# Performance work log

Measured on AMD Instinct MI355X. Metric: run time of the kernel, lower is better.

## Reference

```python
import jax, jax.numpy as jnp
import numpy as np
from jax import lax

B, C, H, W = 4, 256, 64, 64
R1, R2 = 4, 8


def conv1x1(x, w, b):
    # x: [B,C,H,W], w: [O,C], b: [O]
    return jnp.einsum('bchw,oc->bohw', x, w) + b[None, :, None, None]


def dwconv3x3(x, w, b):
    # depthwise 3x3, SAME padding. w: [C,1,3,3]
    y = lax.conv_general_dilated(x, w, window_strides=(1, 1), padding='SAME',
                                 dimension_numbers=('NCHW', 'OIHW', 'NCHW'),
                                 feature_group_count=x.shape[1])
    return y + b[None, :, None, None]


def setup_inputs() -> dict:
    key = jax.random.key(0)
    ks = jax.random.split(key, 20)
    s = 0.02
    inp = {
        'x':   jax.random.normal(ks[0], (B, C, H, W), jnp.float32),
        'Wq':  jax.random.normal(ks[1], (C, C), jnp.float32) * s,
        'bq':  jnp.zeros((C,), jnp.float32),
        'Wk':  jax.random.normal(ks[2], (C, 1, 3, 3), jnp.float32) * s,
        'bk':  jnp.zeros((C,), jnp.float32),
        'Wv':  jax.random.normal(ks[3], (C, 1, 3, 3), jnp.float32) * s,
        'bv':  jnp.zeros((C,), jnp.float32),
        'Wl':  jax.random.normal(ks[4], (C, 1, 3, 3), jnp.float32) * s,
        'bl':  jnp.zeros((C,), jnp.float32),
        'Ws1': jax.random.normal(ks[5], (C // R1, C), jnp.float32) * s,
        'bs1': jnp.zeros((C // R1,), jnp.float32),
        'Ws2': jax.random.normal(ks[6], (C, C // R1), jnp.float32) * s,
        'bs2': jnp.zeros((C,), jnp.float32),
        'Wc1': jax.random.normal(ks[7], (C // R2, C), jnp.float32) * s,
        'bc1': jnp.zeros((C // R2,), jnp.float32),
        'Wc2': jax.random.normal(ks[8], (C, C // R2), jnp.float32) * s,
        'bc2': jnp.zeros((C,), jnp.float32),
        'Wo':  jax.random.normal(ks[9], (C, C), jnp.float32) * s,
        'bo':  jnp.zeros((C,), jnp.float32),
    }
    return inp


def reference(x, Wq, bq, Wk, bk, Wv, bv, Wl, bl, Ws1, bs1, Ws2, bs2,
              Wc1, bc1, Wc2, bc2, Wo, bo):
    b_, c_, h_, w_ = x.shape
    hw = h_ * w_
    scale = jnp.sqrt(jnp.float32(c_))

    q = conv1x1(x, Wq, bq).reshape(b_, c_, hw).transpose(0, 2, 1)   # [B,HW,C]
    k = dwconv3x3(x, Wk, bk).reshape(b_, c_, hw)                    # [B,C,HW]
    v_img = dwconv3x3(x, Wv, bv)                                    # [B,C,H,W]
    v = v_img.reshape(b_, c_, hw).transpose(0, 2, 1)                # [B,HW,C]

    attn = jax.nn.softmax(jnp.einsum('bnc,bcm->bnm', q, k) / scale, axis=-1)
    global_out = jnp.einsum('bnm,bmc->bnc', attn, v)                # [B,HW,C]
    global_out = global_out.transpose(0, 2, 1).reshape(b_, c_, h_, w_)

    local_out = dwconv3x3(v_img, Wl, bl)                            # [B,C,H,W]

    spatial_weight = jax.nn.sigmoid(
        conv1x1(jax.nn.relu(conv1x1(local_out, Ws1, bs1)), Ws2, bs2))

    gap = jnp.mean(global_out, axis=(2, 3), keepdims=True)          # [B,C,1,1]
    channel_weight = jax.nn.sigmoid(
        conv1x1(jax.nn.relu(conv1x1(gap, Wc1, bc1)), Wc2, bc2))     # [B,C,1,1]

    fused = global_out * channel_weight + local_out * spatial_weight
    return conv1x1(fused, Wo, bo) + x
```

## Files before the change

### kernel.cpp

```cpp
#include <hip/hip_runtime.h>
#include <hip/hip_fp8.h>
#include <stdint.h>

typedef unsigned short u16;
typedef unsigned char u8;
typedef __attribute__((ext_vector_type(8))) __bf16 bf16x8;
typedef __attribute__((ext_vector_type(8))) short short8s;
typedef __attribute__((ext_vector_type(4))) float float4v;
typedef __attribute__((ext_vector_type(16))) float floatx16;
typedef __attribute__((ext_vector_type(4))) int int4v;
typedef __attribute__((ext_vector_type(8))) int int8v;

static constexpr int NB = 4, NC = 256, NH = 64, NW = 64, NHW = 4096;
static constexpr int BC = 64;
static constexpr int NKV = 4;
static constexpr int KVCHUNK = NHW / NKV;

static constexpr size_t MB = 1ull << 20;
static constexpr size_t OFF_KBF    = 0;
static constexpr size_t OFF_LBF    = 8 * MB;
static constexpr size_t OFF_GT     = 0;
static constexpr size_t OFF_XT     = 16 * MB;
static constexpr size_t OFF_LPART  = 16 * MB;
static constexpr size_t OFF_FUSEDT = 16 * MB;
static constexpr size_t OFF_QT8    = 24 * MB;
static constexpr size_t OFF_KT8    = 32 * MB;
static constexpr size_t OFF_V8     = 40 * MB;
static constexpr size_t OFF_LT     = 48 * MB;
static constexpr size_t OFF_OPART  = 56 * MB;
static constexpr size_t OFF_HIDT   = 88 * MB;
static constexpr size_t OFF_GAP    = OFF_HIDT + 2 * MB;
static constexpr size_t OFF_WQB    = OFF_GAP + 8 * 1024;
static constexpr size_t OFF_WS1B   = OFF_WQB + 131072;
static constexpr size_t OFF_WS2B   = OFF_WS1B + 32768;
static constexpr size_t OFF_WOB    = OFF_WS2B + 32768;

__device__ __forceinline__ float b2f(u16 h) {
    union { float f; unsigned u; } v; v.u = ((unsigned)h) << 16; return v.f;
}
__device__ __forceinline__ u16 f2b(float f) {
    union { float f; unsigned u; } v; v.f = f;
    unsigned r = v.u + 0x7fffu + ((v.u >> 16) & 1u);
    return (u16)(r >> 16);
}
__device__ __forceinline__ u8 f2f8(float f) {
    __hip_fp8_e4m3 h(f);
    return *reinterpret_cast<u8*>(&h);
}

__device__ __forceinline__ void load_lds16(const void* gsrc, void* ldst) {
    __builtin_amdgcn_global_load_lds(
        (__attribute__((address_space(1))) void*)(uintptr_t)gsrc,
        (__attribute__((address_space(3))) void*)ldst,
        16, 0, 0);
}

__global__ __launch_bounds__(256) void prep(
    const float* __restrict__ x,
    const float* __restrict__ Wq, const float* __restrict__ Ws1,
    const float* __restrict__ Ws2, const float* __restrict__ Wo,
    const float* __restrict__ Wk, const float* __restrict__ bk,
    const float* __restrict__ Wv, const float* __restrict__ bv,
    const float* __restrict__ Wl, const float* __restrict__ bl,
    u16* __restrict__ Wqb, u16* __restrict__ Ws1b, u16* __restrict__ Ws2b, u16* __restrict__ Wob,
    float* __restrict__ gap,
    u16* __restrict__ k_bf, u8* __restrict__ vN8, u16* __restrict__ local_bf,
    u16* __restrict__ xT)
{
    __shared__ __align__(16) unsigned char pshm[9216];
    const int bid = blockIdx.x;
    const int t = threadIdx.x;

    if (bid < 644) {
        int id = bid * 256 + t;
        if (id < 65536)        Wqb[id] = f2b(Wq[id]);
        else if (id < 81920)   Ws1b[id - 65536] = f2b(Ws1[id - 65536]);
        else if (id < 98304)   Ws2b[id - 81920] = f2b(Ws2[id - 81920]);
        else if (id < 163840)  Wob[id - 98304] = f2b(Wo[id - 98304]);
        else if (id < 164864)  gap[id - 163840] = 0.f;
        return;
    }
    if (bid < 2692) {
        int l = bid - 644;
        int xx0 = t & 63, cl = t >> 6;
        int y0 = (l & 7) * 8;
        int c  = ((l >> 3) & 63) * 4 + cl;
        int b  = l >> 9;
        const float* xb = x + ((size_t)b * NC + c) * NHW;
        float wk[9], wv[9], wl[9];
#pragma unroll
        for (int i = 0; i < 9; i++) { wk[i] = Wk[c*9+i]; wv[i] = Wv[c*9+i]; wl[i] = Wl[c*9+i]; }
        float bkc = bk[c], bvc = bv[c], blc = bl[c];

        auto ldx = [&](int y) -> float {
            return ((unsigned)y <= 63u) ? xb[y * 64 + xx0] : 0.f;
        };
        auto conv3 = [&](const float* w9, float a, float bm, float cc) -> float {
            float au = __shfl_up(a, 1, 64),   ad = __shfl_down(a, 1, 64);
            float bu = __shfl_up(bm, 1, 64),  bd = __shfl_down(bm, 1, 64);
            float cu = __shfl_up(cc, 1, 64),  cd = __shfl_down(cc, 1, 64);
            float al = (xx0 == 0) ? 0.f : au, ar = (xx0 == 63) ? 0.f : ad;
            float bl_ = (xx0 == 0) ? 0.f : bu, br = (xx0 == 63) ? 0.f : bd;
            float cle = (xx0 == 0) ? 0.f : cu, cr = (xx0 == 63) ? 0.f : cd;
            return w9[0]*al + w9[1]*a  + w9[2]*ar
                 + w9[3]*bl_ + w9[4]*bm + w9[5]*br
                 + w9[6]*cle + w9[7]*cc + w9[8]*cr;
        };

        float xm2 = ldx(y0 - 2), xm1 = ldx(y0 - 1), x0v = ldx(y0), xp1 = ldx(y0 + 1);
        float vm1 = (y0 - 1 >= 0) ? (bvc + conv3(wv, xm2, xm1, x0v)) : 0.f;
        float v0  = bvc + conv3(wv, xm1, x0v, xp1);

        size_t base = ((size_t)b * NC + c) * NHW;
#pragma unroll
        for (int yi = 0; yi < 8; yi++) {
            int y = y0 + yi;
            float xp2 = ldx(y + 2);
            float vp1 = (y + 1 <= 63) ? (bvc + conv3(wv, x0v, xp1, xp2)) : 0.f;
            float kk  = bkc + conv3(wk, xm1, x0v, xp1);
            float ll  = blc + conv3(wl, vm1, v0, vp1);
            size_t o = base + y * 64 + xx0;
            k_bf[o]     = f2b(kk);
            vN8[o]      = f2f8(v0);
            local_bf[o] = f2b(ll);
            xm1 = x0v; x0v = xp1; xp1 = xp2;
            vm1 = v0;  v0 = vp1;
        }
        return;
    }
    {
        u16 (*tile)[72] = reinterpret_cast<u16 (*)[72]>(pshm);
        int l = bid - 2692;
        int n0 = (l & 63) * 64;
        int c0 = ((l >> 6) & 3) * 64;
        int b  = l >> 8;
        const float* src = x + (size_t)b * NC * NHW;
        u16* dst = xT + (size_t)b * NHW * NC;
        int c = t >> 2, nb = (t & 3) * 16;
#pragma unroll
        for (int q = 0; q < 4; q++) {
            float4 v = *(const float4*)(src + (size_t)(c0 + c) * NHW + n0 + nb + q * 4);
            tile[c][nb + q * 4 + 0] = f2b(v.x);
            tile[c][nb + q * 4 + 1] = f2b(v.y);
            tile[c][nb + q * 4 + 2] = f2b(v.z);
            tile[c][nb + q * 4 + 3] = f2b(v.w);
        }
        __syncthreads();
        int cl = t & 63, ng = t >> 6;
#pragma unroll
        for (int j = 0; j < 16; j++) {
            int n = ng * 16 + j;
            dst[(size_t)(n0 + n) * NC + c0 + cl] = tile[cl][n];
        }
    }
}

__global__ __launch_bounds__(256) void mid(
    const u16* __restrict__ k_bf, const u16* __restrict__ local_bf,
    u8* __restrict__ kT8, u16* __restrict__ localT,
    const u16* __restrict__ xT, const u16* __restrict__ Wqb, const float* __restrict__ bq,
    u8* __restrict__ qT8)
{
    __shared__ __align__(16) u16 tile[64][72];
    const int t = threadIdx.x;
    const int bid = blockIdx.x;
    if (bid < 2048) {
        int n0 = (bid & 63) * 64, c0 = ((bid >> 6) & 3) * 64;
        int zb = bid >> 8, b = zb >> 1;
        const u16* src = (zb & 1) ? local_bf : k_bf;
        src += (size_t)b * NC * NHW;
        int c = t >> 2, nb = (t & 3) * 16;
        *(short8s*)&tile[c][nb]     = *(const short8s*)(src + (size_t)(c0 + c) * NHW + n0 + nb);
        *(short8s*)&tile[c][nb + 8] = *(const short8s*)(src + (size_t)(c0 + c) * NHW + n0 + nb + 8);
        __syncthreads();
        int cl = t & 63, ng = t >> 6;
        if (zb & 1) {
            u16* dst = localT + (size_t)b * NHW * NC;
#pragma unroll
            for (int j = 0; j < 16; j++) {
                int n = ng * 16 + j;
                dst[(size_t)(n0 + n) * NC + c0 + cl] = tile[cl][n];
            }
        } else {
            u8* dst = kT8 + (size_t)b * NHW * NC;
#pragma unroll
            for (int j = 0; j < 16; j++) {
                int n = ng * 16 + j;
                dst[(size_t)(n0 + n) * NC + c0 + cl] = f2f8(b2f(tile[cl][n]));
            }
        }
        return;
    }
    {
        const int w = t >> 6, lane = t & 63;
        const int lm = lane & 15, quad = lane >> 4;
        const int l = bid - 2048;
        const int b = l >> 7;
        const int s_base = (l & 127) * 32 + (w & 1) * 16;
        const int ch = (w >> 1) * 128;
        const u16* xTb = xT + (size_t)b * NHW * NC;
        u8* qTb = qT8 + (size_t)b * NHW * NC;
        bf16x8 aq[8];
#pragma unroll
        for (int kt = 0; kt < 8; kt++)
            aq[kt] = *(const bf16x8*)(xTb + (size_t)(s_base + lm) * NC + kt * 32 + quad * 8);
        float4v acc[8];
#pragma unroll
        for (int j = 0; j < 8; j++) acc[j] = (float4v){0.f, 0.f, 0.f, 0.f};
#pragma unroll
        for (int kt = 0; kt < 8; kt++) {
#pragma unroll
            for (int j = 0; j < 8; j++) {
                bf16x8 bw = *(const bf16x8*)(Wqb + (size_t)(ch + j * 16 + lm) * 256 + kt * 32 + quad * 8);
                acc[j] = __builtin_amdgcn_mfma_f32_16x16x32_bf16(aq[kt], bw, acc[j], 0, 0, 0);
            }
        }
#pragma unroll
        for (int j = 0; j < 8; j++) {
            int cout = ch + j * 16 + lm;
            float bb = bq[cout];
#pragma unroll
            for (int r = 0; r < 4; r++) {
                int s = s_base + quad * 4 + r;
                qTb[(size_t)s * NC + cout] = f2f8(acc[j][r] + bb);
            }
        }
    }
}

__device__ __forceinline__ void stage_tiles(
    const u8* __restrict__ kb, const u8* __restrict__ vb8, int kv0,
    u8* KlB, u8* VlB, int w, int lane)
{
#pragma unroll
    for (int i = 0; i < 4; i++) {
        int g = (w * 4 + i) * 64 + lane;
        int n = g >> 4, jj = g & 15, cc = jj ^ (n & 15);
        load_lds16(kb + (size_t)(kv0 + n) * NC + cc * 16, KlB + (w * 4 + i) * 1024);
    }
#pragma unroll
    for (int i = 0; i < 4; i++) {
        int g = (w * 4 + i) * 64 + lane;
        int c = g >> 2, hh = g & 3;
        int sc = hh ^ ((c >> 1) & 3);
        load_lds16(vb8 + (size_t)c * NHW + kv0 + sc * 16, VlB + (w * 4 + i) * 1024);
    }
}

__global__ __launch_bounds__(256, 2) void attn_hid(
    const u8* __restrict__ qT8, const u8* __restrict__ kT8,
    const u8* __restrict__ vN8, u8* __restrict__ Opart8, float* __restrict__ lpart,
    const u16* __restrict__ localT, const u16* __restrict__ Ws1b, const float* __restrict__ bs1,
    u16* __restrict__ hidT)
{
    __shared__ __align__(16) u8 Kl[2][BC * 256];
    __shared__ __align__(16) u8 Vl[2][256 * BC];

    const int t = threadIdx.x;
    const int w = t >> 6, lane = t & 63;

    if (blockIdx.x >= 512) {
        const int lm = lane & 15, quad = lane >> 4;
        const int l = blockIdx.x - 512;
        const int b = l >> 7;
        const int s_base = (l & 127) * 32 + (w & 1) * 16;
        const int ch = (w >> 1) * 32;
        const u16* lTb = localT + (size_t)b * NHW * NC;
        u16* hTb = hidT + (size_t)b * NHW * 64;
        bf16x8 ah[8];
#pragma unroll
        for (int kt = 0; kt < 8; kt++)
            ah[kt] = *(const bf16x8*)(lTb + (size_t)(s_base + lm) * NC + kt * 32 + quad * 8);
        float4v acc[2];
#pragma unroll
        for (int j = 0; j < 2; j++) acc[j] = (float4v){0.f, 0.f, 0.f, 0.f};
#pragma unroll
        for (int kt = 0; kt < 8; kt++) {
#pragma unroll
            for (int j = 0; j < 2; j++) {
                bf16x8 bw = *(const bf16x8*)(Ws1b + (size_t)(ch + j * 16 + lm) * 256 + kt * 32 + quad * 8);
                acc[j] = __builtin_amdgcn_mfma_f32_16x16x32_bf16(ah[kt], bw, acc[j], 0, 0, 0);
            }
        }
#pragma unroll
        for (int j = 0; j < 2; j++) {
            int h = ch + j * 16 + lm;
            float bb = bs1[h];
#pragma unroll
            for (int r = 0; r < 4; r++) {
                int s = s_base + quad * 4 + r;
                hTb[(size_t)s * 64 + h] = f2b(fmaxf(acc[j][r] + bb, 0.0f));
            }
        }
        return;
    }

    const int combo = blockIdx.x & 15;
    const int b  = combo >> 2;
    const int jc = combo & 3;
    const int n0 = (blockIdx.x >> 4) * 128;
    const int lr = lane & 31, l5 = lane >> 5;
    const int m4 = lr & 15;
    const int scl = (int)0x7F7F7F7F;

    const u8* qb = qT8 + (size_t)b * NHW * NC;
    const u8* kb = kT8 + (size_t)b * NHW * NC;
    const u8* vb8 = vN8 + (size_t)b * NC * NHW;

    int8v aqm[4];
    {
        int qrow = n0 + w * 32 + lr;
#pragma unroll
        for (int ks = 0; ks < 4; ks++)
            aqm[ks] = *(const int8v*)(qb + (size_t)qrow * NC + ks * 64 + l5 * 32);
    }

    floatx16 oacc[8];
#pragma unroll
    for (int i = 0; i < 8; i++)
#pragma unroll
        for (int j = 0; j < 16; j++) oacc[i][j] = 0.f;
    float lsum = 0.f;

    const int kvbeg = jc * KVCHUNK;
    stage_tiles(kb, vb8, kvbeg, Kl[0], Vl[0], w, lane);

    int buf = 0;
#pragma unroll 1
    for (int it = 0; it < KVCHUNK / BC; it++) {
        const int nxt = (it + 1 < KVCHUNK / BC) ? (kvbeg + (it + 1) * BC) : kvbeg;
        stage_tiles(kb, vb8, nxt, Kl[buf ^ 1], Vl[buf ^ 1], w, lane);
        asm volatile("s_waitcnt vmcnt(8)" ::: "memory");
        __builtin_amdgcn_s_barrier();

        const u8* KlB = Kl[buf];
        const u8* VlB = Vl[buf];

        unsigned uA0, uA1, uA2, uA3, uB0, uB1, uB2, uB3;

        {
            floatx16 sacc;
#pragma unroll
            for (int j = 0; j < 16; j++) sacc[j] = 0.f;
            __builtin_amdgcn_s_setprio(1);
#pragma unroll
            for (int ks = 0; ks < 4; ks++) {
                int e = ks * 4 + l5 * 2;
                int4v klo = *(const int4v*)&KlB[lr * 256 + ((e ^ m4) * 16)];
                int4v khi = *(const int4v*)&KlB[lr * 256 + (((e + 1) ^ m4) * 16)];
                int8v ka = __builtin_shufflevector(klo, khi, 0, 1, 2, 3, 4, 5, 6, 7);
                sacc = __builtin_amdgcn_mfma_scale_f32_32x32x64_f8f6f4(
                    ka, aqm[ks], sacc, 0, 0, 0, scl, 0, scl);
            }
            __builtin_amdgcn_s_setprio(0);
            float p[16];
#pragma unroll
            for (int r = 0; r < 16; r++)
                p[r] = __expf(sacc[r] * 0.0625f);
            float s0 = (p[0] + p[1]) + (p[2] + p[3]);
            float s1 = (p[4] + p[5]) + (p[6] + p[7]);
            float s2 = (p[8] + p[9]) + (p[10] + p[11]);
            float s3 = (p[12] + p[13]) + (p[14] + p[15]);
            lsum += (s0 + s1) + (s2 + s3);
            uA0 = __builtin_amdgcn_cvt_pk_fp8_f32(p[0], p[1], 0, false);
            uA0 = __builtin_amdgcn_cvt_pk_fp8_f32(p[2], p[3], uA0, true);
            uA1 = __builtin_amdgcn_cvt_pk_fp8_f32(p[4], p[5], 0, false);
            uA1 = __builtin_amdgcn_cvt_pk_fp8_f32(p[6], p[7], uA1, true);
            uA2 = __builtin_amdgcn_cvt_pk_fp8_f32(p[8], p[9], 0, false);
            uA2 = __builtin_amdgcn_cvt_pk_fp8_f32(p[10], p[11], uA2, true);
            uA3 = __builtin_amdgcn_cvt_pk_fp8_f32(p[12], p[13], 0, false);
            uA3 = __builtin_amdgcn_cvt_pk_fp8_f32(p[14], p[15], uA3, true);
        }
        {
            floatx16 sacc;
#pragma unroll
            for (int j = 0; j < 16; j++) sacc[j] = 0.f;
            __builtin_amdgcn_s_setprio(1);
#pragma unroll
            for (int ks = 0; ks < 4; ks++) {
                int e = ks * 4 + l5 * 2;
                int4v klo = *(const int4v*)&KlB[(32 + lr) * 256 + ((e ^ m4) * 16)];
                int4v khi = *(const int4v*)&KlB[(32 + lr) * 256 + (((e + 1) ^ m4) * 16)];
                int8v ka = __builtin_shufflevector(klo, khi, 0, 1, 2, 3, 4, 5, 6, 7);
                sacc = __builtin_amdgcn_mfma_scale_f32_32x32x64_f8f6f4(
                    ka, aqm[ks], sacc, 0, 0, 0, scl, 0, scl);
            }
            __builtin_amdgcn_s_setprio(0);
            float p[16];
#pragma unroll
            for (int r = 0; r < 16; r++)
                p[r] = __expf(sacc[r] * 0.0625f);
            float s0 = (p[0] + p[1]) + (p[2] + p[3]);
            float s1 = (p[4] + p[5]) + (p[6] + p[7]);
            float s2 = (p[8] + p[9]) + (p[10] + p[11]);
            float s3 = (p[12] + p[13]) + (p[14] + p[15]);
            lsum += (s0 + s1) + (s2 + s3);
            uB0 = __builtin_amdgcn_cvt_pk_fp8_f32(p[0], p[1], 0, false);
            uB0 = __builtin_amdgcn_cvt_pk_fp8_f32(p[2], p[3], uB0, true);
            uB1 = __builtin_amdgcn_cvt_pk_fp8_f32(p[4], p[5], 0, false);
            uB1 = __builtin_amdgcn_cvt_pk_fp8_f32(p[6], p[7], uB1, true);
            uB2 = __builtin_amdgcn_cvt_pk_fp8_f32(p[8], p[9], 0, false);
            uB2 = __builtin_amdgcn_cvt_pk_fp8_f32(p[10], p[11], uB2, true);
            uB3 = __builtin_amdgcn_cvt_pk_fp8_f32(p[12], p[13], 0, false);
            uB3 = __builtin_amdgcn_cvt_pk_fp8_f32(p[14], p[15], uB3, true);
        }
        asm volatile("v_permlane32_swap_b32 %0, %1" : "+v"(uA0), "+v"(uB0));
        asm volatile("v_permlane32_swap_b32 %0, %1" : "+v"(uA1), "+v"(uB1));
        asm volatile("v_permlane32_swap_b32 %0, %1" : "+v"(uA2), "+v"(uB2));
        asm volatile("v_permlane32_swap_b32 %0, %1" : "+v"(uA3), "+v"(uB3));
        int8v pa = {(int)uA0, (int)uB0, (int)uA1, (int)uB1,
                    (int)uA2, (int)uB2, (int)uA3, (int)uB3};

        __builtin_amdgcn_s_setprio(1);
#pragma unroll
        for (int ct = 0; ct < 8; ct++) {
            int c = ct * 32 + lr;
            int sw = (c >> 1) & 3;
            int4v v0 = *(const int4v*)&VlB[c * 64 + (((l5 * 2) ^ sw) * 16)];
            int4v v1 = *(const int4v*)&VlB[c * 64 + (((l5 * 2 + 1) ^ sw) * 16)];
            int8v bv = __builtin_shufflevector(v0, v1, 0, 1, 2, 3, 4, 5, 6, 7);
            oacc[ct] = __builtin_amdgcn_mfma_scale_f32_32x32x64_f8f6f4(
                pa, bv, oacc[ct], 0, 0, 0, scl, 0, scl);
        }
        __builtin_amdgcn_s_setprio(0);
        __builtin_amdgcn_s_barrier();
        buf ^= 1;
    }

    lsum += __shfl_xor(lsum, 32, 64);
    u8* Ob = Opart8 + ((size_t)(b * NKV + jc) * NHW + n0 + w * 32) * NC;
#pragma unroll
    for (int reg = 0; reg < 16; reg++) {
        int row = (reg & 3) + 8 * (reg >> 2) + 4 * l5;
#pragma unroll
        for (int ct = 0; ct < 8; ct++)
            Ob[(size_t)row * NC + ct * 32 + lr] = f2f8(oacc[ct][reg]);
    }
    if (lane < 32)
        lpart[(size_t)(b * NKV + jc) * NHW + n0 + w * 32 + lr] = lsum;
}

__global__ __launch_bounds__(256) void attn_combine(
    const u8* __restrict__ Opart8, const float* __restrict__ lpart,
    u16* __restrict__ gT, float* __restrict__ gap)
{
    __shared__ float gsum[256];
    int t = threadIdx.x;
    gsum[t] = 0.f;
    __syncthreads();
    int b = blockIdx.y;
    int n = blockIdx.x * 8 + (t >> 5);
    int c0 = (t & 31) * 8;
    float acc[8] = {};
    float l = 0.f;
#pragma unroll
    for (int j = 0; j < NKV; j++) {
        const u8* op = Opart8 + ((size_t)(b * NKV + j) * NHW + n) * NC + c0;
        unsigned long long v = *(const unsigned long long*)op;
        unsigned lo = (unsigned)v, hi = (unsigned)(v >> 32);
        acc[0] += __builtin_amdgcn_cvt_f32_fp8(lo, 0);
        acc[1] += __builtin_amdgcn_cvt_f32_fp8(lo, 1);
        acc[2] += __builtin_amdgcn_cvt_f32_fp8(lo, 2);
        acc[3] += __builtin_amdgcn_cvt_f32_fp8(lo, 3);
        acc[4] += __builtin_amdgcn_cvt_f32_fp8(hi, 0);
        acc[5] += __builtin_amdgcn_cvt_f32_fp8(hi, 1);
        acc[6] += __builtin_amdgcn_cvt_f32_fp8(hi, 2);
        acc[7] += __builtin_amdgcn_cvt_f32_fp8(hi, 3);
        l += lpart[(size_t)(b * NKV + j) * NHW + n];
    }
    float inv = 1.0f / l;
#pragma unroll
    for (int i = 0; i < 8; i++) acc[i] *= inv;
    short8s vo;
#pragma unroll
    for (int i = 0; i < 8; i++) ((u16*)&vo)[i] = f2b(acc[i]);
    *(short8s*)(gT + ((size_t)b * NHW + n) * NC + c0) = vo;
#pragma unroll
    for (int i = 0; i < 8; i++) atomicAdd(&gsum[c0 + i], acc[i]);
    __syncthreads();
    atomicAdd(&gap[b * NC + t], gsum[t]);
}

__global__ __launch_bounds__(256) void gemm_swfused_mfma(
    const u16* __restrict__ hidT, const u16* __restrict__ Ws2b, const float* __restrict__ bs2,
    const u16* __restrict__ gT, const u16* __restrict__ localT,
    const float* __restrict__ gap,
    const float* __restrict__ Wc1, const float* __restrict__ bc1,
    const float* __restrict__ Wc2, const float* __restrict__ bc2,
    u16* __restrict__ fusedT)
{
    __shared__ float g[256], h1[32], cwl[256];
    __shared__ float ph[32][9];
    const int t = threadIdx.x, w = t >> 6, lane = t & 63;
    const int lm = lane & 15, quad = lane >> 4;
    const int b = blockIdx.y;

    g[t] = gap[b * 256 + t] * (1.0f / 4096.0f);
    __syncthreads();
    {
        int h = t & 31, part = t >> 5;
        float s = 0.f;
        for (int c = part * 32; c < part * 32 + 32; c++) s += Wc1[h * 256 + c] * g[c];
        ph[h][part] = s;
    }
    __syncthreads();
    if (t < 32) {
        float s = bc1[t];
#pragma unroll
        for (int p = 0; p < 8; p++) s += ph[t][p];
        h1[t] = fmaxf(s, 0.f);
    }
    __syncthreads();
    {
        float s = bc2[t];
#pragma unroll
        for (int j = 0; j < 32; j++) s += Wc2[t * 32 + j] * h1[j];
        cwl[t] = 1.0f / (1.0f + __expf(-s));
    }
    __syncthreads();

    const int s_base = blockIdx.x * 32 + (w & 1) * 16;
    const int ch = (w >> 1) * 128;
    const u16* hTb = hidT + (size_t)b * NHW * 64;
    const u16* lTb = localT + (size_t)b * NHW * NC;
    const u16* gTb = gT + (size_t)b * NHW * NC;
    u16* fTb = fusedT + (size_t)b * NHW * NC;

    bf16x8 aq[2];
#pragma unroll
    for (int kt = 0; kt < 2; kt++)
        aq[kt] = *(const bf16x8*)(hTb + (size_t)(s_base + lm) * 64 + kt * 32 + quad * 8);

    float4v acc[8];
#pragma unroll
    for (int j = 0; j < 8; j++) acc[j] = (float4v){0.f, 0.f, 0.f, 0.f};

#pragma unroll
    for (int kt = 0; kt < 2; kt++) {
#pragma unroll
        for (int j = 0; j < 8; j++) {
            bf16x8 bw = *(const bf16x8*)(Ws2b + (size_t)(ch + j * 16 + lm) * 64 + kt * 32 + quad * 8);
            acc[j] = __builtin_amdgcn_mfma_f32_16x16x32_bf16(aq[kt], bw, acc[j], 0, 0, 0);
        }
    }
#pragma unroll
    for (int j = 0; j < 8; j++) {
        int c = ch + j * 16 + lm;
        float bb = bs2[c];
        float cwv = cwl[c];
#pragma unroll
        for (int r = 0; r < 4; r++) {
            int s = s_base + quad * 4 + r;
            float sw = 1.0f / (1.0f + __expf(-(acc[j][r] + bb)));
            float gg = b2f(gTb[(size_t)s * NC + c]);
            float lo = b2f(lTb[(size_t)s * NC + c]);
            fTb[(size_t)s * NC + c] = f2b(gg * cwv + lo * sw);
        }
    }
}

__global__ __launch_bounds__(256) void gemm_out_mfma(
    const u16* __restrict__ Wob, const u16* __restrict__ fusedT, const float* __restrict__ bo,
    const float* __restrict__ x, float* __restrict__ out)
{
    const int t = threadIdx.x, w = t >> 6, lane = t & 63;
    const int lm = lane & 15, quad = lane >> 4;
    const int b = blockIdx.z;
    const int o_base = blockIdx.x * 32 + (w & 1) * 16;
    const int n_base = blockIdx.y * 256 + (w >> 1) * 128;
    const u16* fTb = fusedT + (size_t)b * NHW * NC;

    bf16x8 aw[8];
#pragma unroll
    for (int kt = 0; kt < 8; kt++)
        aw[kt] = *(const bf16x8*)(Wob + (size_t)(o_base + lm) * 256 + kt * 32 + quad * 8);

    float4v acc[8];
#pragma unroll
    for (int j = 0; j < 8; j++) acc[j] = (float4v){0.f, 0.f, 0.f, 0.f};

#pragma unroll
    for (int kt = 0; kt < 8; kt++) {
#pragma unroll
        for (int j = 0; j < 8; j++) {
            bf16x8 bf = *(const bf16x8*)(fTb + (size_t)(n_base + j * 16 + lm) * NC + kt * 32 + quad * 8);
            acc[j] = __builtin_amdgcn_mfma_f32_16x16x32_bf16(aw[kt], bf, acc[j], 0, 0, 0);
        }
    }
#pragma unroll
    for (int r = 0; r < 4; r++) {
        int o = o_base + quad * 4 + r;
        float bb = bo[o];
        size_t rowoff = ((size_t)b * NC + o) * NHW;
#pragma unroll
        for (int j = 0; j < 8; j++) {
            int n = n_base + j * 16 + lm;
            out[rowoff + n] = acc[j][r] + bb + x[rowoff + n];
        }
    }
}

extern "C" void kernel_launch(void* const* d_in, const int* in_sizes, int n_in,
                              void* d_out, int out_size, void* d_ws, size_t ws_size,
                              hipStream_t stream)
{
    const float* x   = (const float*)d_in[0];
    const float* Wq  = (const float*)d_in[1];
    const float* bq  = (const float*)d_in[2];
    const float* Wk  = (const float*)d_in[3];
    const float* bk  = (const float*)d_in[4];
    const float* Wv  = (const float*)d_in[5];
    const float* bv  = (const float*)d_in[6];
    const float* Wl  = (const float*)d_in[7];
    const float* bl  = (const float*)d_in[8];
    const float* Ws1 = (const float*)d_in[9];
    const float* bs1 = (const float*)d_in[10];
    const float* Ws2 = (const float*)d_in[11];
    const float* bs2 = (const float*)d_in[12];
    const float* Wc1 = (const float*)d_in[13];
    const float* bc1 = (const float*)d_in[14];
    const float* Wc2 = (const float*)d_in[15];
    const float* bc2 = (const float*)d_in[16];
    const float* Wo  = (const float*)d_in[17];
    const float* bo  = (const float*)d_in[18];
    float* out = (float*)d_out;

    char* ws = (char*)d_ws;
    u16* k_bf     = (u16*)(ws + OFF_KBF);
    u16* local_bf = (u16*)(ws + OFF_LBF);
    u16* gT       = (u16*)(ws + OFF_GT);
    u16* xT       = (u16*)(ws + OFF_XT);
    u16* fusedT   = (u16*)(ws + OFF_FUSEDT);
    u8*  qT8      = (u8*)(ws + OFF_QT8);
    u8*  kT8      = (u8*)(ws + OFF_KT8);
    u8*  vN8      = (u8*)(ws + OFF_V8);
    u16* localT   = (u16*)(ws + OFF_LT);
    u8*  Opart8   = (u8*)(ws + OFF_OPART);
    float* lpart  = (float*)(ws + OFF_LPART);
    u16* hidT     = (u16*)(ws + OFF_HIDT);
    float* gap    = (float*)(ws + OFF_GAP);
    u16* Wqb      = (u16*)(ws + OFF_WQB);
    u16* Ws1b     = (u16*)(ws + OFF_WS1B);
    u16* Ws2b     = (u16*)(ws + OFF_WS2B);
    u16* Wob      = (u16*)(ws + OFF_WOB);

    prep<<<dim3(3716), 256, 0, stream>>>(x, Wq, Ws1, Ws2, Wo, Wk, bk, Wv, bv, Wl, bl,
                                         Wqb, Ws1b, Ws2b, Wob, gap, k_bf, vN8, local_bf, xT);
    mid<<<dim3(2560), 256, 0, stream>>>(k_bf, local_bf, kT8, localT, xT, Wqb, bq, qT8);
    attn_hid<<<dim3(1024), 256, 0, stream>>>(qT8, kT8, vN8, Opart8, lpart,
                                             localT, Ws1b, bs1, hidT);
    attn_combine<<<dim3(NHW / 8, 4), 256, 0, stream>>>(Opart8, lpart, gT, gap);
    gemm_swfused_mfma<<<dim3(128, 4), 256, 0, stream>>>(hidT, Ws2b, bs2, gT, localT,
                                                        gap, Wc1, bc1, Wc2, bc2, fusedT);
    gemm_out_mfma<<<dim3(8, 16, 4), 256, 0, stream>>>(Wob, fusedT, bo, x, out);
}
```

Baseline: 259.9 us.

## Fuse gating kernel with output projection via shared-memory fused tile

Result: faster. 247.7 us (median of 2 runs) (-4.7%).

```diff
diff --git a/kernel.cpp b/kernel.cpp
--- a/kernel.cpp
+++ b/kernel.cpp
@@ -22,7 +22,6 @@
 static constexpr size_t OFF_GT     = 0;
 static constexpr size_t OFF_XT     = 16 * MB;
 static constexpr size_t OFF_LPART  = 16 * MB;
-static constexpr size_t OFF_FUSEDT = 16 * MB;
 static constexpr size_t OFF_QT8    = 24 * MB;
 static constexpr size_t OFF_KT8    = 32 * MB;
 static constexpr size_t OFF_V8     = 40 * MB;
@@ -481,16 +480,18 @@
     atomicAdd(&gap[b * NC + t], gsum[t]);
 }
 
-__global__ __launch_bounds__(256) void gemm_swfused_mfma(
+__global__ __launch_bounds__(256) void gemm_tail(
     const u16* __restrict__ hidT, const u16* __restrict__ Ws2b, const float* __restrict__ bs2,
     const u16* __restrict__ gT, const u16* __restrict__ localT,
     const float* __restrict__ gap,
     const float* __restrict__ Wc1, const float* __restrict__ bc1,
     const float* __restrict__ Wc2, const float* __restrict__ bc2,
-    u16* __restrict__ fusedT)
+    const u16* __restrict__ Wob, const float* __restrict__ bo,
+    const float* __restrict__ x, float* __restrict__ out)
 {
     __shared__ float g[256], h1[32], cwl[256];
     __shared__ float ph[32][9];
+    __shared__ __align__(16) u16 fsh[32][264];
     const int t = threadIdx.x, w = t >> 6, lane = t & 63;
     const int lm = lane & 15, quad = lane >> 4;
     const int b = blockIdx.y;
@@ -524,78 +525,77 @@
     const u16* hTb = hidT + (size_t)b * NHW * 64;
     const u16* lTb = localT + (size_t)b * NHW * NC;
     const u16* gTb = gT + (size_t)b * NHW * NC;
-    u16* fTb = fusedT + (size_t)b * NHW * NC;
-
-    bf16x8 aq[2];
-#pragma unroll
-    for (int kt = 0; kt < 2; kt++)
-        aq[kt] = *(const bf16x8*)(hTb + (size_t)(s_base + lm) * 64 + kt * 32 + quad * 8);
-
-    float4v acc[8];
-#pragma unroll
-    for (int j = 0; j < 8; j++) acc[j] = (float4v){0.f, 0.f, 0.f, 0.f};
-
-#pragma unroll
-    for (int kt = 0; kt < 2; kt++) {
+
+    {
+        bf16x8 ah[2];
+#pragma unroll
+        for (int kt = 0; kt < 2; kt++)
+            ah[kt] = *(const bf16x8*)(hTb + (size_t)(s_base + lm) * 64 + kt * 32 + quad * 8);
+
+        float4v acc[8];
+#pragma unroll
+        for (int j = 0; j < 8; j++) acc[j] = (float4v){0.f, 0.f, 0.f, 0.f};
+
+#pragma unroll
+        for (int kt = 0; kt < 2; kt++) {
+#pragma unroll
+            for (int j = 0; j < 8; j++) {
+                bf16x8 bw = *(const bf16x8*)(Ws2b + (size_t)(ch + j * 16 + lm) * 64 + kt * 32 + quad * 8);
+                acc[j] = __builtin_amdgcn_mfma_f32_16x16x32_bf16(ah[kt], bw, acc[j], 0, 0, 0);
+            }
+        }
 #pragma unroll
         for (int j = 0; j < 8; j++) {
-            bf16x8 bw = *(const bf16x8*)(Ws2b + (size_t)(ch + j * 16 + lm) * 64 + kt * 32 + quad * 8);
-            acc[j] = __builtin_amdgcn_mfma_f32_16x16x32_bf16(aq[kt], bw, acc[j], 0, 0, 0);
-        }
-    }
-#pragma unroll
-    for (int j = 0; j < 8; j++) {
-        int c = ch + j * 16 + lm;
-        float bb = bs2[c];
-        float cwv = cwl[c];
-#pragma unroll
-        for (int r = 0; r < 4; r++) {
-            int s = s_base + quad * 4 + r;
-            float sw = 1.0f / (1.0f + __expf(-(acc[j][r] + bb)));
-            float gg = b2f(gTb[(size_t)s * NC + c]);
-            float lo = b2f(lTb[(size_t)s * NC + c]);
-            fTb[(size_t)s * NC + c] = f2b(gg * cwv + lo * sw);
-        }
-    }
-}
-
-__global__ __launch_bounds__(256) void gemm_out_mfma(
-    const u16* __restrict__ Wob, const u16* __restrict__ fusedT, const float* __restrict__ bo,
-    const float* __restrict__ x, float* __restrict__ out)
-{
-    const int t = threadIdx.x, w = t >> 6, lane = t & 63;
-    const int lm = lane & 15, quad = lane >> 4;
-    const int b = blockIdx.z;
-    const int o_base = blockIdx.x * 32 + (w & 1) * 16;
-    const int n_base = blockIdx.y * 256 + (w >> 1) * 128;
-    const u16* fTb = fusedT + (size_t)b * NHW * NC;
-
-    bf16x8 aw[8];
-#pragma unroll
-    for (int kt = 0; kt < 8; kt++)
-        aw[kt] = *(const bf16x8*)(Wob + (size_t)(o_base + lm) * 256 + kt * 32 + quad * 8);
-
-    float4v acc[8];
-#pragma unroll
-    for (int j = 0; j < 8; j++) acc[j] = (float4v){0.f, 0.f, 0.f, 0.f};
-
-#pragma unroll
-    for (int kt = 0; kt < 8; kt++) {
-#pragma unroll
-        for (int j = 0; j < 8; j++) {
-            bf16x8 bf = *(const bf16x8*)(fTb + (size_t)(n_base + j * 16 + lm) * NC + kt * 32 + quad * 8);
-            acc[j] = __builtin_amdgcn_mfma_f32_16x16x32_bf16(aw[kt], bf, acc[j], 0, 0, 0);
-        }
-    }
-#pragma unroll
-    for (int r = 0; r < 4; r++) {
-        int o = o_base + quad * 4 + r;
-        float bb = bo[o];
-        size_t rowoff = ((size_t)b * NC + o) * NHW;
-#pragma unroll
-        for (int j = 0; j < 8; j++) {
-            int n = n_base + j * 16 + lm;
-            out[rowoff + n] = acc[j][r] + bb + x[rowoff + n];
+            int c = ch + j * 16 + lm;
+            float bb = bs2[c];
+            float cwv = cwl[c];
+#pragma unroll
+            for (int r = 0; r < 4; r++) {
+                int s = s_base + quad * 4 + r;
+                int srow = (w & 1) * 16 + quad * 4 + r;
+                float sw = 1.0f / (1.0f + __expf(-(acc[j][r] + bb)));
+                float gg = b2f(gTb[(size_t)s * NC + c]);
+                float lo = b2f(lTb[(size_t)s * NC + c]);
+                fsh[srow][c] = f2b(gg * cwv + lo * sw);
+            }
+        }
+    }
+    __syncthreads();
+
+    {
+        const int n_glob = blockIdx.x * 32;
+        const int o_base = w * 64;
+        float4v acc[4][2];
+#pragma unroll
+        for (int oj = 0; oj < 4; oj++)
+#pragma unroll
+            for (int nj = 0; nj < 2; nj++) acc[oj][nj] = (float4v){0.f, 0.f, 0.f, 0.f};
+
+#pragma unroll
+        for (int kt = 0; kt < 8; kt++) {
+#pragma unroll
+            for (int oj = 0; oj < 4; oj++) {
+                bf16x8 aw = *(const bf16x8*)(Wob + (size_t)(o_base + oj * 16 + lm) * 256 + kt * 32 + quad * 8);
+#pragma unroll
+                for (int nj = 0; nj < 2; nj++) {
+                    bf16x8 bf = *(const bf16x8*)&fsh[nj * 16 + lm][kt * 32 + quad * 8];
+                    acc[oj][nj] = __builtin_amdgcn_mfma_f32_16x16x32_bf16(aw, bf, acc[oj][nj], 0, 0, 0);
+                }
+            }
+        }
+#pragma unroll
+        for (int oj = 0; oj < 4; oj++) {
+#pragma unroll
+            for (int r = 0; r < 4; r++) {
+                int o = o_base + oj * 16 + quad * 4 + r;
+                float bb = bo[o];
+                size_t rowoff = ((size_t)b * NC + o) * NHW;
+#pragma unroll
+                for (int nj = 0; nj < 2; nj++) {
+                    int n = n_glob + nj * 16 + lm;
+                    out[rowoff + n] = acc[oj][nj][r] + bb + x[rowoff + n];
+                }
+            }
         }
     }
 }
@@ -630,7 +630,6 @@
     u16* local_bf = (u16*)(ws + OFF_LBF);
     u16* gT       = (u16*)(ws + OFF_GT);
     u16* xT       = (u16*)(ws + OFF_XT);
-    u16* fusedT   = (u16*)(ws + OFF_FUSEDT);
     u8*  qT8      = (u8*)(ws + OFF_QT8);
     u8*  kT8      = (u8*)(ws + OFF_KT8);
     u8*  vN8      = (u8*)(ws + OFF_V8);
@@ -650,7 +649,7 @@
     attn_hid<<<dim3(1024), 256, 0, stream>>>(qT8, kT8, vN8, Opart8, lpart,
                                              localT, Ws1b, bs1, hidT);
     attn_combine<<<dim3(NHW / 8, 4), 256, 0, stream>>>(Opart8, lpart, gT, gap);
-    gemm_swfused_mfma<<<dim3(128, 4), 256, 0, stream>>>(hidT, Ws2b, bs2, gT, localT,
-                                                        gap, Wc1, bc1, Wc2, bc2, fusedT);
-    gemm_out_mfma<<<dim3(8, 16, 4), 256, 0, stream>>>(Wob, fusedT, bo, x, out);
-}
+    gemm_tail<<<dim3(128, 4), 256, 0, stream>>>(hidT, Ws2b, bs2, gT, localT,
+                                                gap, Wc1, bc1, Wc2, bc2,
+                                                Wob, bo, x, out);
+}
```
